# Performance work log

Measured on AMD Instinct MI355X. Metric: run time of the kernel, lower is better.

## Reference

```python
import jax, jax.numpy as jnp
import numpy as np

DIM = 256          # dim_m == dim_d (required by hist @ W1)
HIST = 200         # history_num
B = 2048
U_TOT = 100000
V_TOT = 100000
EPS = 1e-12


def _max_norm_lookup(table, idx):
    # torch nn.Embedding(max_norm=1): rows are renormalized to L2 norm <= 1 at lookup.
    g = table[idx]
    n = jnp.linalg.norm(g, axis=-1, keepdims=True)
    return g * jnp.minimum(1.0, 1.0 / jnp.maximum(n, EPS))


def _l2norm(x):
    # F.normalize(x, 2, -1)
    return x / jnp.maximum(jnp.linalg.norm(x, axis=-1, keepdims=True), EPS)


def setup_inputs() -> dict:
    key = jax.random.key(0)
    ks = jax.random.split(key, 12)
    xav = float(np.sqrt(6.0 / (DIM + DIM)))
    xav_pb = float(np.sqrt(6.0 / (HIST + DIM)))
    return {
        "batch_u": jax.random.randint(ks[0], (B,), 0, U_TOT),
        "batch_v": jax.random.randint(ks[1], (B,), 0, V_TOT),
        "batch_history": jax.random.randint(ks[2], (B, HIST), 0, V_TOT),
        "batch_olc": jax.random.randint(ks[3], (B,), 0, 68),
        "batch_cluster_olc": jax.random.randint(ks[4], (B,), 0, 68),
        "user_emb": jax.random.normal(ks[5], (U_TOT, DIM), jnp.float32),
        "venue_emb": jax.random.normal(ks[6], (V_TOT, DIM), jnp.float32),
        "W1": jax.random.uniform(ks[7], (DIM, DIM), jnp.float32, -xav, xav),
        "W2": jax.random.uniform(ks[8], (DIM, DIM), jnp.float32, -xav, xav),
        "P": jax.random.normal(ks[9], (HIST, DIM), jnp.float32),
        "bias": jax.random.uniform(ks[10], (HIST, DIM), jnp.float32, -xav_pb, xav_pb),
        "a": jax.random.normal(ks[11], (1,), jnp.float32),
    }


def reference(batch_u, batch_v, batch_history, batch_olc, batch_cluster_olc,
              user_emb, venue_emb, W1, W2, P, bias, a):
    # batch_olc / batch_cluster_olc are read but unused in the original forward.
    u = _max_norm_lookup(user_emb, batch_u)            # [B, D]
    v = _max_norm_lookup(venue_emb, batch_v)           # [B, D]
    hist = _max_norm_lookup(venue_emb, batch_history)  # [B, H, D]

    # h = tanh(hist @ W1 + (P @ W2) + bias), broadcast over batch
    h = jnp.tanh(jnp.einsum('bhd,de->bhe', hist, W1) + (P @ W2)[None] + bias[None])
    alpha = jax.nn.softmax(h, axis=1)                  # softmax over history dim
    l = jnp.sum(alpha * hist, axis=1) + a              # [B, D], scalar a broadcast

    # TransE-style score with p_norm = 2
    s = _l2norm(u) + _l2norm(l) - _l2norm(v)
    return jnp.sqrt(jnp.sum(s * s, axis=-1))           # [B]
```

## Files before the change

### kernel.cpp

```cpp
#include <hip/hip_runtime.h>

#define DIM 256
#define HIST 200
#define MPAD 208
#define BATCH 2048
#define HSTRIDE 264
#define EPSF 1e-12f

typedef __bf16 bf16x8 __attribute__((ext_vector_type(8)));
typedef float f32x4 __attribute__((ext_vector_type(4)));

__device__ __forceinline__ unsigned short f2bf(float f) {
    union { float f; unsigned u; } v; v.f = f;
    unsigned r = (v.u + 0x7fffu + ((v.u >> 16) & 1u)) >> 16;
    return (unsigned short)r;
}
__device__ __forceinline__ float bf2f(unsigned short u) {
    union { unsigned u; float f; } v; v.u = ((unsigned)u) << 16;
    return v.f;
}

__global__ __launch_bounds__(256) void k_vscale(const float* __restrict__ venue,
                                                float* __restrict__ sInv, int nrows) {
    const int row = blockIdx.x * 4 + (threadIdx.x >> 6);
    if (row >= nrows) return;
    const int lane = threadIdx.x & 63;
    const float4 g = *(const float4*)(venue + (size_t)row * DIM + lane * 4);
    float ss = g.x * g.x + g.y * g.y + g.z * g.z + g.w * g.w;
#pragma unroll
    for (int off = 32; off > 0; off >>= 1) ss += __shfl_xor(ss, off);
    if (lane == 0) sInv[row] = fminf(1.f, 1.f / fmaxf(sqrtf(ss), EPSF));
}

__global__ __launch_bounds__(256) void k_w1t(const float* __restrict__ W1,
                                             unsigned short* __restrict__ W1t) {
    __shared__ float tile[64][65];
    const int bi = blockIdx.x >> 2;
    const int bj = blockIdx.x & 3;
    const int tid = threadIdx.x;
#pragma unroll
    for (int it = 0; it < 16; ++it) {
        int idx = tid + it * 256;
        int r = idx >> 6, c = idx & 63;
        tile[r][c] = W1[(bi * 64 + r) * DIM + bj * 64 + c];
    }
    __syncthreads();
#pragma unroll
    for (int it = 0; it < 16; ++it) {
        int idx = tid + it * 256;
        int c = idx >> 6, r = idx & 63;
        W1t[(bj * 64 + c) * DIM + bi * 64 + r] = f2bf(tile[r][c]);
    }
}

__global__ __launch_bounds__(256) void k_Ct(const float* __restrict__ P,
                                            const float* __restrict__ W2,
                                            const float* __restrict__ bias,
                                            float* __restrict__ Ct) {
    __shared__ float Prow[DIM];
    const int h = blockIdx.x, e = threadIdx.x;
    Prow[e] = P[h * DIM + e];
    __syncthreads();
    float acc = bias[h * DIM + e];
#pragma unroll 8
    for (int d = 0; d < DIM; ++d) acc += Prow[d] * W2[d * DIM + e];
    Ct[e * MPAD + h] = acc;
}

__global__ __launch_bounds__(256, 1) void k_main(
    const int* __restrict__ batch_u, const int* __restrict__ batch_v,
    const int* __restrict__ batch_history,
    const float* __restrict__ user_emb, const float* __restrict__ venue_emb,
    const float* __restrict__ Ct, const unsigned short* __restrict__ W1t,
    const float* __restrict__ sInv,
    const float* __restrict__ a_ptr, float* __restrict__ out) {

    __shared__ unsigned short histS[MPAD * HSTRIDE];
    __shared__ float scaleS[MPAD];
    __shared__ int idxS[MPAD];
    __shared__ float lArr[DIM];
    __shared__ float redS[4][4];
    __shared__ float invS[4];

    const int b = blockIdx.x;
    const int tid = threadIdx.x;
    const int wave = tid >> 6;
    const int lane = tid & 63;
    const int quad = lane >> 4;
    const int l16 = lane & 15;
    const int ncol0 = wave * 64 + l16 * 4;

    if (tid < MPAD) {
        int m = (tid < HIST) ? tid : 0;
        int ix = batch_history[b * HIST + m];
        idxS[tid] = ix;
        scaleS[tid] = sInv[ix];
    }
    __syncthreads();

    f32x4 acc[13][4];
#pragma unroll
    for (int mt = 0; mt < 13; ++mt)
#pragma unroll
        for (int i = 0; i < 4; ++i)
            acc[mt][i] = *(const f32x4*)(Ct + (ncol0 + i) * MPAD + mt * 16 + quad * 4);

    const int r0 = wave * 52;
    float4 buf[8];
#pragma unroll
    for (int j = 0; j < 8; ++j)
        buf[j] = *(const float4*)(venue_emb + (size_t)idxS[r0 + j] * DIM + lane * 4);
#pragma unroll
    for (int j = 0; j < 52; ++j) {
        float4 g = buf[j % 8];
        if (j + 8 < 52)
            buf[j % 8] = *(const float4*)(venue_emb + (size_t)idxS[r0 + j + 8] * DIM + lane * 4);
        float s = scaleS[r0 + j];
        ushort4 pk = { f2bf(g.x * s), f2bf(g.y * s), f2bf(g.z * s), f2bf(g.w * s) };
        *(ushort4*)&histS[(r0 + j) * HSTRIDE + lane * 4] = pk;
    }
    __syncthreads();

    const float ut = user_emb[(size_t)batch_u[b] * DIM + tid];
    const float vt = venue_emb[(size_t)batch_v[b] * DIM + tid];

#pragma unroll
    for (int k = 0; k < 8; ++k) {
        bf16x8 Bf[4];
#pragma unroll
        for (int i = 0; i < 4; ++i) {
            int n = ncol0 + i;
            Bf[i] = *(const bf16x8*)(const void*)(W1t + n * DIM + k * 32 + quad * 8);
        }
#pragma unroll
        for (int mt = 0; mt < 13; ++mt) {
            const bf16x8 Af =
                *(const bf16x8*)(const void*)(&histS[(mt * 16 + l16) * HSTRIDE + k * 32 + quad * 8]);
#pragma unroll
            for (int i = 0; i < 4; ++i)
                acc[mt][i] = __builtin_amdgcn_mfma_f32_16x16x32_bf16(Af, Bf[i], acc[mt][i], 0, 0, 0);
        }
    }

    const float a_val = a_ptr[0];
    float Ssum[4] = {0.f, 0.f, 0.f, 0.f};
    float Lnum[4] = {0.f, 0.f, 0.f, 0.f};
#pragma unroll
    for (int mt = 0; mt < 13; ++mt)
#pragma unroll
        for (int r = 0; r < 4; ++r) {
            int m = mt * 16 + quad * 4 + r;
            if (m < HIST) {
                ushort4 hv = *(const ushort4*)&histS[m * HSTRIDE + ncol0];
                float hw[4] = { bf2f(hv.x), bf2f(hv.y), bf2f(hv.z), bf2f(hv.w) };
#pragma unroll
                for (int i = 0; i < 4; ++i) {
                    float x = acc[mt][i][r];
                    float e2 = __expf(2.f * x);
                    float th = 1.f - 2.f / (e2 + 1.f);
                    float e = __expf(th);
                    Ssum[i] += e;
                    Lnum[i] += e * hw[i];
                }
            }
        }
#pragma unroll
    for (int i = 0; i < 4; ++i) {
        Ssum[i] += __shfl_xor(Ssum[i], 16); Ssum[i] += __shfl_xor(Ssum[i], 32);
        Lnum[i] += __shfl_xor(Lnum[i], 16); Lnum[i] += __shfl_xor(Lnum[i], 32);
        if (quad == 0) lArr[ncol0 + i] = Lnum[i] / Ssum[i] + a_val;
    }
    __syncthreads();

    const float lt = lArr[tid];
    float pu = ut * ut, pv = vt * vt, pl = lt * lt;
#pragma unroll
    for (int off = 32; off > 0; off >>= 1) {
        pu += __shfl_xor(pu, off);
        pv += __shfl_xor(pv, off);
        pl += __shfl_xor(pl, off);
    }
    if (lane == 0) { redS[wave][0] = pu; redS[wave][1] = pv; redS[wave][2] = pl; }
    __syncthreads();
    if (tid == 0) {
        float su = 0.f, sv = 0.f, sl = 0.f;
        for (int w = 0; w < 4; ++w) { su += redS[w][0]; sv += redS[w][1]; sl += redS[w][2]; }
        invS[0] = 1.f / fmaxf(sqrtf(su), EPSF);
        invS[1] = 1.f / fmaxf(sqrtf(sv), EPSF);
        invS[2] = 1.f / fmaxf(sqrtf(sl), EPSF);
    }
    __syncthreads();
    float s = ut * invS[0] + lt * invS[2] - vt * invS[1];
    float s2 = s * s;
#pragma unroll
    for (int off = 32; off > 0; off >>= 1) s2 += __shfl_xor(s2, off);
    if (lane == 0) redS[wave][3] = s2;
    __syncthreads();
    if (tid == 0) out[b] = sqrtf(redS[0][3] + redS[1][3] + redS[2][3] + redS[3][3]);
}

extern "C" void kernel_launch(void* const* d_in, const int* in_sizes, int n_in,
                              void* d_out, int out_size, void* d_ws, size_t ws_size,
                              hipStream_t stream) {
    const int* batch_u = (const int*)d_in[0];
    const int* batch_v = (const int*)d_in[1];
    const int* batch_history = (const int*)d_in[2];
    const float* user_emb = (const float*)d_in[5];
    const float* venue_emb = (const float*)d_in[6];
    const float* W1 = (const float*)d_in[7];
    const float* W2 = (const float*)d_in[8];
    const float* P = (const float*)d_in[9];
    const float* bias = (const float*)d_in[10];
    const float* a = (const float*)d_in[11];
    float* out = (float*)d_out;

    const int nV = in_sizes[6] / DIM;

    float* Ct = (float*)d_ws;
    unsigned short* W1t = (unsigned short*)((char*)d_ws + 212992);
    float* sInv = (float*)((char*)d_ws + 212992 + 131072);

    k_vscale<<<(nV + 3) / 4, 256, 0, stream>>>(venue_emb, sInv, nV);
    k_w1t<<<16, 256, 0, stream>>>(W1, W1t);
    k_Ct<<<HIST, 256, 0, stream>>>(P, W2, bias, Ct);
    k_main<<<BATCH, 256, 0, stream>>>(batch_u, batch_v, batch_history,
                                      user_emb, venue_emb, Ct, W1t, sInv, a, out);
}
```

Measured before the change: 470.1 us.

## Use 1024-thread blocks in main kernel and merge prep kernels into one

The main kernel moves from 256 to 1024 threads per block. Each of 16 waves now computes one 16-column N tile instead of four, which cuts the accumulators per thread from 52 to 13 vectors and lets the history gather be spread over more waves. W1t and Ct are written in fragment-friendly layouts so each lane's MFMA operand and accumulator init are contiguous loads. The three preprocessing kernels are merged into one launch to save launch overhead. In exchange, 16 waves share one block's LDS and barriers, and occupancy now depends on the 4-blocks-per-CU launch bound together with LDS use.

```diff
diff --git a/kernel.cpp b/kernel.cpp
--- a/kernel.cpp
+++ b/kernel.cpp
@@ -20,58 +20,51 @@
     return v.f;
 }
 
-__global__ __launch_bounds__(256) void k_vscale(const float* __restrict__ venue,
-                                                float* __restrict__ sInv, int nrows) {
-    const int row = blockIdx.x * 4 + (threadIdx.x >> 6);
-    if (row >= nrows) return;
-    const int lane = threadIdx.x & 63;
-    const float4 g = *(const float4*)(venue + (size_t)row * DIM + lane * 4);
-    float ss = g.x * g.x + g.y * g.y + g.z * g.z + g.w * g.w;
-#pragma unroll
-    for (int off = 32; off > 0; off >>= 1) ss += __shfl_xor(ss, off);
-    if (lane == 0) sInv[row] = fminf(1.f, 1.f / fmaxf(sqrtf(ss), EPSF));
-}
-
-__global__ __launch_bounds__(256) void k_w1t(const float* __restrict__ W1,
-                                             unsigned short* __restrict__ W1t) {
-    __shared__ float tile[64][65];
-    const int bi = blockIdx.x >> 2;
-    const int bj = blockIdx.x & 3;
-    const int tid = threadIdx.x;
-#pragma unroll
-    for (int it = 0; it < 16; ++it) {
-        int idx = tid + it * 256;
-        int r = idx >> 6, c = idx & 63;
-        tile[r][c] = W1[(bi * 64 + r) * DIM + bj * 64 + c];
-    }
-    __syncthreads();
-#pragma unroll
-    for (int it = 0; it < 16; ++it) {
-        int idx = tid + it * 256;
-        int c = idx >> 6, r = idx & 63;
-        W1t[(bj * 64 + c) * DIM + bi * 64 + r] = f2bf(tile[r][c]);
-    }
-}
-
-__global__ __launch_bounds__(256) void k_Ct(const float* __restrict__ P,
-                                            const float* __restrict__ W2,
-                                            const float* __restrict__ bias,
-                                            float* __restrict__ Ct) {
-    __shared__ float Prow[DIM];
-    const int h = blockIdx.x, e = threadIdx.x;
-    Prow[e] = P[h * DIM + e];
-    __syncthreads();
-    float acc = bias[h * DIM + e];
+__global__ __launch_bounds__(256) void k_prep(
+    const float* __restrict__ W1, const float* __restrict__ P,
+    const float* __restrict__ W2, const float* __restrict__ bias,
+    const float* __restrict__ venue,
+    unsigned short* __restrict__ W1t2, float* __restrict__ Ct2,
+    float* __restrict__ sInv, int nV) {
+    const int bid = blockIdx.x, tid = threadIdx.x;
+    if (bid < 16) {
+#pragma unroll
+        for (int it = 0; it < 16; ++it) {
+            int idx = bid * 4096 + it * 256 + tid;
+            int g = idx >> 11, rem = idx & 2047;
+            int n = rem >> 3, j = rem & 7;
+            W1t2[idx] = f2bf(W1[(g * 8 + j) * DIM + n]);
+        }
+    } else if (bid < 224) {
+        const int h = bid - 16;
+        __shared__ float Prow[DIM];
+        const int e = tid;
+        float acc = 0.f;
+        if (h < HIST) {
+            Prow[e] = P[h * DIM + e];
+            __syncthreads();
+            acc = bias[h * DIM + e];
 #pragma unroll 8
-    for (int d = 0; d < DIM; ++d) acc += Prow[d] * W2[d * DIM + e];
-    Ct[e * MPAD + h] = acc;
-}
-
-__global__ __launch_bounds__(256, 1) void k_main(
+            for (int d = 0; d < DIM; ++d) acc += Prow[d] * W2[d * DIM + e];
+        }
+        Ct2[((h >> 4) * 4 + ((h >> 2) & 3)) * 1024 + e * 4 + (h & 3)] = acc;
+    } else {
+        const int row = (bid - 224) * 4 + (tid >> 6);
+        if (row >= nV) return;
+        const int lane = tid & 63;
+        const float4 g = *(const float4*)(venue + (size_t)row * DIM + lane * 4);
+        float ss = g.x * g.x + g.y * g.y + g.z * g.z + g.w * g.w;
+#pragma unroll
+        for (int off = 32; off > 0; off >>= 1) ss += __shfl_xor(ss, off);
+        if (lane == 0) sInv[row] = fminf(1.f, 1.f / fmaxf(sqrtf(ss), EPSF));
+    }
+}
+
+__global__ __launch_bounds__(1024, 4) void k_main(
     const int* __restrict__ batch_u, const int* __restrict__ batch_v,
     const int* __restrict__ batch_history,
     const float* __restrict__ user_emb, const float* __restrict__ venue_emb,
-    const float* __restrict__ Ct, const unsigned short* __restrict__ W1t,
+    const float* __restrict__ Ct2, const unsigned short* __restrict__ W1t2,
     const float* __restrict__ sInv,
     const float* __restrict__ a_ptr, float* __restrict__ out) {
 
@@ -80,7 +73,7 @@
     __shared__ int idxS[MPAD];
     __shared__ float lArr[DIM];
     __shared__ float redS[4][4];
-    __shared__ float invS[4];
+    __shared__ float invS[3];
 
     const int b = blockIdx.x;
     const int tid = threadIdx.x;
@@ -88,7 +81,7 @@
     const int lane = tid & 63;
     const int quad = lane >> 4;
     const int l16 = lane & 15;
-    const int ncol0 = wave * 64 + l16 * 4;
+    const int n = wave * 16 + l16;
 
     if (tid < MPAD) {
         int m = (tid < HIST) ? tid : 0;
@@ -98,81 +91,64 @@
     }
     __syncthreads();
 
-    f32x4 acc[13][4];
+    const int r0 = wave * 13;
+    float4 buf[13];
+#pragma unroll
+    for (int j = 0; j < 13; ++j)
+        buf[j] = *(const float4*)(venue_emb + (size_t)idxS[r0 + j] * DIM + lane * 4);
+#pragma unroll
+    for (int j = 0; j < 13; ++j) {
+        float s = scaleS[r0 + j];
+        ushort4 pk = { f2bf(buf[j].x * s), f2bf(buf[j].y * s),
+                       f2bf(buf[j].z * s), f2bf(buf[j].w * s) };
+        *(ushort4*)&histS[(r0 + j) * HSTRIDE + lane * 4] = pk;
+    }
+
+    f32x4 acc[13];
 #pragma unroll
     for (int mt = 0; mt < 13; ++mt)
-#pragma unroll
-        for (int i = 0; i < 4; ++i)
-            acc[mt][i] = *(const f32x4*)(Ct + (ncol0 + i) * MPAD + mt * 16 + quad * 4);
-
-    const int r0 = wave * 52;
-    float4 buf[8];
-#pragma unroll
-    for (int j = 0; j < 8; ++j)
-        buf[j] = *(const float4*)(venue_emb + (size_t)idxS[r0 + j] * DIM + lane * 4);
-#pragma unroll
-    for (int j = 0; j < 52; ++j) {
-        float4 g = buf[j % 8];
-        if (j + 8 < 52)
-            buf[j % 8] = *(const float4*)(venue_emb + (size_t)idxS[r0 + j + 8] * DIM + lane * 4);
-        float s = scaleS[r0 + j];
-        ushort4 pk = { f2bf(g.x * s), f2bf(g.y * s), f2bf(g.z * s), f2bf(g.w * s) };
-        *(ushort4*)&histS[(r0 + j) * HSTRIDE + lane * 4] = pk;
-    }
-    __syncthreads();
-
-    const float ut = user_emb[(size_t)batch_u[b] * DIM + tid];
-    const float vt = venue_emb[(size_t)batch_v[b] * DIM + tid];
+        acc[mt] = *(const f32x4*)(Ct2 + (mt * 4 + quad) * 1024 + n * 4);
+
+    float ut = 0.f, vt = 0.f;
+    if (tid < DIM) {
+        ut = user_emb[(size_t)batch_u[b] * DIM + tid];
+        vt = venue_emb[(size_t)batch_v[b] * DIM + tid];
+    }
+    __syncthreads();
 
 #pragma unroll
     for (int k = 0; k < 8; ++k) {
-        bf16x8 Bf[4];
-#pragma unroll
-        for (int i = 0; i < 4; ++i) {
-            int n = ncol0 + i;
-            Bf[i] = *(const bf16x8*)(const void*)(W1t + n * DIM + k * 32 + quad * 8);
-        }
+        const bf16x8 Bf = *(const bf16x8*)(const void*)(W1t2 + (k * 4 + quad) * 2048 + n * 8);
 #pragma unroll
         for (int mt = 0; mt < 13; ++mt) {
             const bf16x8 Af =
                 *(const bf16x8*)(const void*)(&histS[(mt * 16 + l16) * HSTRIDE + k * 32 + quad * 8]);
-#pragma unroll
-            for (int i = 0; i < 4; ++i)
-                acc[mt][i] = __builtin_amdgcn_mfma_f32_16x16x32_bf16(Af, Bf[i], acc[mt][i], 0, 0, 0);
+            acc[mt] = __builtin_amdgcn_mfma_f32_16x16x32_bf16(Af, Bf, acc[mt], 0, 0, 0);
         }
     }
 
     const float a_val = a_ptr[0];
-    float Ssum[4] = {0.f, 0.f, 0.f, 0.f};
-    float Lnum[4] = {0.f, 0.f, 0.f, 0.f};
+    float Ssum = 0.f, Lnum = 0.f;
 #pragma unroll
     for (int mt = 0; mt < 13; ++mt)
 #pragma unroll
         for (int r = 0; r < 4; ++r) {
             int m = mt * 16 + quad * 4 + r;
             if (m < HIST) {
-                ushort4 hv = *(const ushort4*)&histS[m * HSTRIDE + ncol0];
-                float hw[4] = { bf2f(hv.x), bf2f(hv.y), bf2f(hv.z), bf2f(hv.w) };
-#pragma unroll
-                for (int i = 0; i < 4; ++i) {
-                    float x = acc[mt][i][r];
-                    float e2 = __expf(2.f * x);
-                    float th = 1.f - 2.f / (e2 + 1.f);
-                    float e = __expf(th);
-                    Ssum[i] += e;
-                    Lnum[i] += e * hw[i];
-                }
+                float x = acc[mt][r];
+                float e2 = __expf(2.f * x);
+                float th = 1.f - 2.f / (e2 + 1.f);
+                float e = __expf(th);
+                Ssum += e;
+                Lnum += e * bf2f(histS[m * HSTRIDE + n]);
             }
         }
-#pragma unroll
-    for (int i = 0; i < 4; ++i) {
-        Ssum[i] += __shfl_xor(Ssum[i], 16); Ssum[i] += __shfl_xor(Ssum[i], 32);
-        Lnum[i] += __shfl_xor(Lnum[i], 16); Lnum[i] += __shfl_xor(Lnum[i], 32);
-        if (quad == 0) lArr[ncol0 + i] = Lnum[i] / Ssum[i] + a_val;
-    }
-    __syncthreads();
-
-    const float lt = lArr[tid];
+    Ssum += __shfl_xor(Ssum, 16); Ssum += __shfl_xor(Ssum, 32);
+    Lnum += __shfl_xor(Lnum, 16); Lnum += __shfl_xor(Lnum, 32);
+    if (quad == 0) lArr[n] = Lnum / Ssum + a_val;
+    __syncthreads();
+
+    const float lt = (tid < DIM) ? lArr[tid] : 0.f;
     float pu = ut * ut, pv = vt * vt, pl = lt * lt;
 #pragma unroll
     for (int off = 32; off > 0; off >>= 1) {
@@ -180,7 +156,7 @@
         pv += __shfl_xor(pv, off);
         pl += __shfl_xor(pl, off);
     }
-    if (lane == 0) { redS[wave][0] = pu; redS[wave][1] = pv; redS[wave][2] = pl; }
+    if (lane == 0 && wave < 4) { redS[wave][0] = pu; redS[wave][1] = pv; redS[wave][2] = pl; }
     __syncthreads();
     if (tid == 0) {
         float su = 0.f, sv = 0.f, sl = 0.f;
@@ -194,7 +170,7 @@
     float s2 = s * s;
 #pragma unroll
     for (int off = 32; off > 0; off >>= 1) s2 += __shfl_xor(s2, off);
-    if (lane == 0) redS[wave][3] = s2;
+    if (lane == 0 && wave < 4) redS[wave][3] = s2;
     __syncthreads();
     if (tid == 0) out[b] = sqrtf(redS[0][3] + redS[1][3] + redS[2][3] + redS[3][3]);
 }
@@ -216,13 +192,12 @@
 
     const int nV = in_sizes[6] / DIM;
 
-    float* Ct = (float*)d_ws;
-    unsigned short* W1t = (unsigned short*)((char*)d_ws + 212992);
+    float* Ct2 = (float*)d_ws;
+    unsigned short* W1t2 = (unsigned short*)((char*)d_ws + 212992);
     float* sInv = (float*)((char*)d_ws + 212992 + 131072);
 
-    k_vscale<<<(nV + 3) / 4, 256, 0, stream>>>(venue_emb, sInv, nV);
-    k_w1t<<<16, 256, 0, stream>>>(W1, W1t);
-    k_Ct<<<HIST, 256, 0, stream>>>(P, W2, bias, Ct);
-    k_main<<<BATCH, 256, 0, stream>>>(batch_u, batch_v, batch_history,
-                                      user_emb, venue_emb, Ct, W1t, sInv, a, out);
-}
+    k_prep<<<224 + (nV + 3) / 4, 256, 0, stream>>>(W1, P, W2, bias, venue_emb,
+                                                   W1t2, Ct2, sInv, nV);
+    k_main<<<BATCH, 1024, 0, stream>>>(batch_u, batch_v, batch_history,
+                                       user_emb, venue_emb, Ct2, W1t2, sInv, a, out);
+}
```

Result: faster. 413.1 us (-12.1%).
